# Kernel optimization log

Hardware: AMD Instinct MI355X
Metric: run time of the kernel (lower is better)

The kernel has to match this reference:

```python
import math
import jax, jax.numpy as jnp
import numpy as np

N_TOKENS = 2048
HIDDEN = 2880
HEAD_DIM = 64
N_HEADS = 64          # total attention heads
N_KV = 8              # key/value heads
Q_MULT = N_HEADS // N_KV
SLIDING_WINDOW = 128  # layer_idx=0 (even) -> window active
ROPE_BASE = 150000.0
INIT_CTX = 4096.0
ROPE_SCALE = 32.0
NTK_ALPHA = 1.0
NTK_BETA = 32.0
QKV_DIM = HEAD_DIM * (N_HEADS + 2 * N_KV)  # 5120
EPS = 1e-5
NEG = -1e30


def _cos_sin(n_tokens):
    # YaRN-scaled rotary tables (scaling_factor > 1 branch)
    freq = ROPE_BASE ** (jnp.arange(0, HEAD_DIM, 2, dtype=jnp.float32) / HEAD_DIM)
    concentration = 0.1 * jnp.log(jnp.float32(ROPE_SCALE)) + 1.0
    d_half = HEAD_DIM / 2
    log_base = jnp.log(jnp.float32(ROPE_BASE))
    low = d_half * jnp.log(jnp.float32(INIT_CTX / (NTK_BETA * 2 * np.pi))) / log_base
    high = d_half * jnp.log(jnp.float32(INIT_CTX / (NTK_ALPHA * 2 * np.pi))) / log_base
    interpolation = 1.0 / (ROPE_SCALE * freq)
    extrapolation = 1.0 / freq
    ramp = (jnp.arange(d_half, dtype=jnp.float32) - low) / (high - low)
    mask = 1.0 - jnp.clip(ramp, 0.0, 1.0)
    inv_freq = interpolation * (1.0 - mask) + extrapolation * mask
    t = jnp.arange(n_tokens, dtype=jnp.float32)
    freqs = t[:, None] * inv_freq[None, :]          # [n, head_dim//2]
    return jnp.cos(freqs) * concentration, jnp.sin(freqs) * concentration


def _apply_rotary(x, cos, sin):
    # x: [n, heads, head_dim]; cos/sin: [n, head_dim//2]
    cos = cos[:, None, :].astype(x.dtype)
    sin = sin[:, None, :].astype(x.dtype)
    x1, x2 = jnp.split(x, 2, axis=-1)
    return jnp.concatenate((x1 * cos - x2 * sin, x2 * cos + x1 * sin), axis=-1)


def _rmsnorm(x, scale):
    t = x.astype(jnp.float32)
    rms = jnp.sqrt(jnp.mean(t * t, axis=-1, keepdims=True) + EPS)
    return (t / rms * scale).astype(x.dtype)


def _sdpa(q, k, v, sinks):
    # q: [n, h_kv, q_mult, d]; k, v: [n, h_kv, d]; sinks: [n_heads]
    n = q.shape[0]
    sm_scale = 1.0 / math.sqrt(HEAD_DIM)
    q32, k32, v32 = q.astype(jnp.float32), k.astype(jnp.float32), v.astype(jnp.float32)
    qk = jnp.einsum('qhmd,khd->hmqk', q32, k32) * jnp.float32(sm_scale)
    i = jnp.arange(n)
    # causal AND within sliding window: q - window < k <= q
    allowed = (i[None, :] <= i[:, None]) & (i[None, :] > i[:, None] - SLIDING_WINDOW)
    qk = qk + jnp.where(allowed, jnp.float32(0.0), jnp.float32(NEG))[None, None, :, :]
    s = sinks.astype(jnp.float32).reshape(N_KV, Q_MULT, 1, 1)
    s = jnp.broadcast_to(s, (N_KV, Q_MULT, n, 1))
    w = jax.nn.softmax(jnp.concatenate([qk, s], axis=-1), axis=-1)[..., :-1]
    attn = jnp.einsum('hmqk,khd->qhmd', w, v32)
    return attn.astype(q.dtype).reshape(n, -1)  # [n, n_heads*head_dim]


def setup_inputs() -> dict:
    key = jax.random.key(0)
    ks = jax.random.split(key, 5)
    s = 0.02
    return {
        'x': jax.random.normal(ks[0], (N_TOKENS, HIDDEN), jnp.float32),
        'norm_scale': jnp.ones((HIDDEN,), jnp.float32),
        'w_qkv': jax.random.normal(ks[1], (HIDDEN, QKV_DIM), jnp.float32) * s,
        'b_qkv': jnp.zeros((QKV_DIM,), jnp.float32),
        'sinks': jax.random.normal(ks[2], (N_HEADS,), jnp.float32),
        'w_out': jax.random.normal(ks[3], (N_HEADS * HEAD_DIM, HIDDEN), jnp.float32) * s,
        'b_out': jnp.zeros((HIDDEN,), jnp.float32),
    }


def reference(x, norm_scale, w_qkv, b_qkv, sinks, w_out, b_out):
    n = x.shape[0]
    t = _rmsnorm(x, norm_scale)
    qkv = t @ w_qkv + b_qkv                                   # [n, qkv_dim]
    q_end = N_HEADS * HEAD_DIM
    k_end = q_end + N_KV * HEAD_DIM
    q = qkv[:, :q_end].reshape(n, N_KV, Q_MULT, HEAD_DIM)
    k = qkv[:, q_end:k_end].reshape(n, N_KV, HEAD_DIM)
    v = qkv[:, k_end:].reshape(n, N_KV, HEAD_DIM)
    cos, sin = _cos_sin(n)
    q = _apply_rotary(q.reshape(n, -1, HEAD_DIM), cos, sin).reshape(n, N_KV, Q_MULT, HEAD_DIM)
    k = _apply_rotary(k, cos, sin)
    attn = _sdpa(q, k, v, sinks)                              # [n, n_heads*head_dim]
    return x + (attn @ w_out + b_out)
```

## Files before the change

### kernel.cpp

```cpp
#include <hip/hip_runtime.h>
#include <hip/hip_bf16.h>
#include <math.h>

#define N_TOK 2048
#define HIDDEN 2880
#define QKV_DIM 5120
#define LOG2E 1.44269504088896340736f

typedef __attribute__((ext_vector_type(8))) short short8;
typedef __attribute__((ext_vector_type(4))) float f32x4;
typedef __attribute__((ext_vector_type(16))) float f32x16;

__device__ __forceinline__ float bf2f(unsigned short u) {
  union { unsigned int i; float f; } c; c.i = ((unsigned int)u) << 16; return c.f;
}
__device__ __forceinline__ unsigned short f2bf(float f) {
  union { float f; unsigned int i; } c; c.f = f;
  unsigned int i = c.i;
  return (unsigned short)((i + 0x7FFFu + ((i >> 16) & 1u)) >> 16);
}
__device__ __forceinline__ void gload16(const void* g, void* l) {
  __builtin_amdgcn_global_load_lds((const __attribute__((address_space(1))) void*)g,
                                   (__attribute__((address_space(3))) void*)l, 16, 0, 0);
}

__global__ __launch_bounds__(256) void prep_kernel(
    const float* __restrict__ w_qkv, unsigned short* __restrict__ wqkvT,
    const float* __restrict__ w_out, unsigned short* __restrict__ woutT,
    const float* __restrict__ x, const float* __restrict__ scale,
    unsigned short* __restrict__ t_bf,
    float* __restrict__ cstab, float* __restrict__ sntab)
{
  __shared__ float tile[64][65];
  int b = blockIdx.x;
  const int t = threadIdx.x;
  if (b >= 8528) {
    const float log_base = 11.9183905731f;
    const float low  = 32.f * logf(4096.f / (32.f * 6.283185307179586f)) / log_base;
    const float high = 32.f * logf(4096.f / 6.283185307179586f) / log_base;
    const float conc = 1.3465735903f;
    int e0 = (b - 8528) * 1024 + t * 4;
#pragma unroll
    for (int k = 0; k < 4; ++k) {
      int entry = e0 + k;
      int token = entry >> 5, d = entry & 31;
      float fj = (float)d;
      float extrap = expf(-log_base * fj * 0.03125f);
      float interp = extrap * 0.03125f;
      float ramp = (fj - low) / (high - low);
      float maskv = 1.f - fminf(fmaxf(ramp, 0.f), 1.f);
      float inv_freq = interp * (1.f - maskv) + extrap * maskv;
      float ang = (float)token * inv_freq;
      float s, c;
      sincosf(ang, &s, &c);
      cstab[entry] = c * conc;
      sntab[entry] = s * conc;
    }
    return;
  }
  if (b >= 6480) {
    int row = b - 6480;
    const float* xr = x + (size_t)row * HIDDEN;
    float ss = 0.f;
    for (int i = t; i < HIDDEN / 4; i += 256) {
      float4 v = ((const float4*)xr)[i];
      ss += v.x * v.x + v.y * v.y + v.z * v.z + v.w * v.w;
    }
#pragma unroll
    for (int off = 32; off; off >>= 1) ss += __shfl_down(ss, off, 64);
    __shared__ float red[4];
    if ((t & 63) == 0) red[t >> 6] = ss;
    __syncthreads();
    float total = red[0] + red[1] + red[2] + red[3];
    float rinv = rsqrtf(total / (float)HIDDEN + 1e-5f);
    for (int i = t; i < HIDDEN / 4; i += 256) {
      float4 v = ((const float4*)xr)[i];
      float4 s4 = ((const float4*)scale)[i];
      union { unsigned short u[4]; uint2 p; } pk;
      pk.u[0] = f2bf(v.x * rinv * s4.x);
      pk.u[1] = f2bf(v.y * rinv * s4.y);
      pk.u[2] = f2bf(v.z * rinv * s4.z);
      pk.u[3] = f2bf(v.w * rinv * s4.w);
      *(uint2*)&t_bf[(size_t)row * HIDDEN + i * 4] = pk.p;
    }
    return;
  }
  const float* in; unsigned short* out; int R, C, bx, by;
  if (b < 3600) { in = w_qkv; out = wqkvT; R = 2880; C = 5120; bx = b % 80; by = b / 80; }
  else { b -= 3600; in = w_out; out = woutT; R = 4096; C = 2880; bx = b % 45; by = b / 45; }
  const int r0 = by * 64, c0 = bx * 64;
  const int c4 = t & 15, rr = t >> 4;
#pragma unroll
  for (int p = 0; p < 4; ++p) {
    int row = rr + p * 16;
    float4 v = *(const float4*)&in[(size_t)(r0 + row) * C + c0 + c4 * 4];
    tile[row][c4 * 4 + 0] = v.x; tile[row][c4 * 4 + 1] = v.y;
    tile[row][c4 * 4 + 2] = v.z; tile[row][c4 * 4 + 3] = v.w;
  }
  __syncthreads();
  const int rc = t & 7;
#pragma unroll
  for (int it = 0; it < 2; ++it) {
    int cc = (t >> 3) + it * 32;
    unsigned short tmp[8];
#pragma unroll
    for (int i = 0; i < 8; ++i) tmp[i] = f2bf(tile[rc * 8 + i][cc]);
    *(uint4*)&out[(size_t)(c0 + cc) * R + r0 + rc * 8] = *(uint4*)tmp;
  }
}

template <int NF, int EPI>
__global__ __launch_bounds__(512, 2) void gemm8(
    const unsigned short* __restrict__ A,
    const unsigned short* __restrict__ Bt,
    const float* __restrict__ bias,
    const float* __restrict__ resid,
    void* __restrict__ Cout,
    int K, int Ncols)
{
  constexpr int BUFSZ = 16384 + NF * 8192;
  constexpr int NCH = 2 + NF;
  constexpr int HALF = NCH / 2;
  __shared__ char smem_[2 * BUFSZ];
  const int tid = threadIdx.x;
  const int lane = tid & 63;
  const int w = tid >> 6;
  const int fr = lane & 15, fq = lane >> 4;
  const int wr = w >> 2, wc = w & 3;

  const int nwg = gridDim.x;
  const int cpx = nwg >> 3;
  const int wg = (blockIdx.x & 7) * cpx + (blockIdx.x >> 3);
  const int by = wg & 15, bx = wg >> 4;
  const int row0 = by * 128, col0 = bx * (NF * 64);

  const unsigned short* gsrc[NCH];
  int ldsoff[NCH];
#pragma unroll
  for (int c = 0; c < NCH; ++c) {
    int g = tid + 512 * c;
    if (g < 1024) {
      int kk = g >> 9, rr = (g >> 2) & 127, u = g & 3;
      gsrc[c] = A + (size_t)(row0 + rr) * K + kk * 32 + ((u ^ ((rr >> 1) & 3)) * 8);
      ldsoff[c] = kk * 8192 + rr * 64 + u * 16;
    } else {
      int g2 = g - 1024;
      int kk = g2 / (NF * 256);
      int rm = g2 - kk * (NF * 256);
      int rr = rm >> 2, u = rm & 3;
      gsrc[c] = Bt + (size_t)(col0 + rr) * K + kk * 32 + ((u ^ ((rr >> 1) & 3)) * 8);
      ldsoff[c] = 16384 + kk * (NF * 4096) + rr * 64 + u * 16;
    }
  }
  const int urd = (fq ^ ((fr >> 1) & 3)) * 16;
  const int aoffb = (wr * 64 + fr) * 64 + urd;
  const int boffb = 16384 + (wc * NF * 16 + fr) * 64 + urd;

  f32x4 acc[4][NF];
#pragma unroll
  for (int mf = 0; mf < 4; ++mf)
#pragma unroll
    for (int nf = 0; nf < NF; ++nf) acc[mf][nf] = (f32x4)0.f;

  const int NT = K >> 6;

#define ISSUE(c) gload16(gsrc[c] + ktn, smem_ + nbufo + ldsoff[c])
#define RD_A(mf, kk) (*(const short8*)(smem_ + bufo + (kk)*8192 + (mf)*1024 + aoffb))
#define RD_B(nf, kk) (*(const short8*)(smem_ + bufo + (kk)*(NF*4096) + (nf)*1024 + boffb))

  {
    const int ktn = 0, nbufo = 0;
#pragma unroll
    for (int c = 0; c < NCH; ++c) gload16(gsrc[c] + ktn, smem_ + nbufo + ldsoff[c]);
  }

  for (int t = 0; t < NT; ++t) {
    const int bufo = (t & 1) * BUFSZ;
    const int nbufo = bufo ^ BUFSZ;
    const int ktn = (t + 1) * 64;
    const bool pref = (t + 1) < NT;

    asm volatile("s_waitcnt vmcnt(0)" ::: "memory");
    __builtin_amdgcn_s_barrier();

    if (pref) {
#pragma unroll
      for (int c = 0; c < HALF; ++c) ISSUE(c);
    }

    short8 afr[4], bfr[NF];
#pragma unroll
    for (int nf = 0; nf < NF; ++nf) bfr[nf] = RD_B(nf, 0);
#pragma unroll
    for (int mf = 0; mf < 4; ++mf) afr[mf] = RD_A(mf, 0);
    __builtin_amdgcn_s_setprio(1);
#pragma unroll
    for (int mf = 0; mf < 4; ++mf)
#pragma unroll
      for (int nf = 0; nf < NF; ++nf)
        acc[mf][nf] = __builtin_amdgcn_mfma_f32_16x16x32_bf16(afr[mf], bfr[nf], acc[mf][nf], 0, 0, 0);
    __builtin_amdgcn_s_setprio(0);

    if (pref) {
#pragma unroll
      for (int c = HALF; c < NCH; ++c) ISSUE(c);
    }

#pragma unroll
    for (int nf = 0; nf < NF; ++nf) bfr[nf] = RD_B(nf, 1);
#pragma unroll
    for (int mf = 0; mf < 4; ++mf) afr[mf] = RD_A(mf, 1);
    __builtin_amdgcn_s_setprio(1);
#pragma unroll
    for (int mf = 0; mf < 4; ++mf)
#pragma unroll
      for (int nf = 0; nf < NF; ++nf)
        acc[mf][nf] = __builtin_amdgcn_mfma_f32_16x16x32_bf16(afr[mf], bfr[nf], acc[mf][nf], 0, 0, 0);
    __builtin_amdgcn_s_setprio(0);
  }
#undef ISSUE
#undef RD_A
#undef RD_B

#pragma unroll
  for (int mf = 0; mf < 4; ++mf) {
#pragma unroll
    for (int nf = 0; nf < NF; ++nf) {
      const int colb = col0 + wc * NF * 16 + nf * 16 + fr;
      const int rowb = row0 + wr * 64 + mf * 16 + fq * 4;
      const float bs = bias[colb];
      if (EPI == 1) {
#pragma unroll
        for (int j = 0; j < 4; ++j)
          ((unsigned short*)Cout)[(size_t)(rowb + j) * Ncols + colb] =
              f2bf(acc[mf][nf][j] + bs);
      } else {
#pragma unroll
        for (int j = 0; j < 4; ++j) {
          const size_t idx = (size_t)(rowb + j) * Ncols + colb;
          ((float*)Cout)[idx] = acc[mf][nf][j] + bs + resid[idx];
        }
      }
    }
  }
}

__global__ __launch_bounds__(512, 2) void gemm_d3(
    const unsigned short* __restrict__ A,
    const unsigned short* __restrict__ Bt,
    const float* __restrict__ bias,
    const float* __restrict__ resid,
    float* __restrict__ Cout,
    int K, int Ncols)
{
  constexpr int NF = 3;
  constexpr int BUFSZ = 16384 + NF * 8192;
  constexpr int NCH = 2 + NF;
  __shared__ char smem_[3 * BUFSZ];
  const int tid = threadIdx.x;
  const int lane = tid & 63;
  const int w = tid >> 6;
  const int fr = lane & 15, fq = lane >> 4;
  const int wr = w >> 2, wc = w & 3;

  const int nwg = gridDim.x;
  const int cpx = nwg >> 3;
  const int wg = (blockIdx.x & 7) * cpx + (blockIdx.x >> 3);
  const int by = wg & 15, bx = wg >> 4;
  const int row0 = by * 128, col0 = bx * (NF * 64);

  const unsigned short* gsrc[NCH];
  int ldsoff[NCH];
#pragma unroll
  for (int c = 0; c < NCH; ++c) {
    int g = tid + 512 * c;
    if (g < 1024) {
      int kk = g >> 9, rr = (g >> 2) & 127, u = g & 3;
      gsrc[c] = A + (size_t)(row0 + rr) * K + kk * 32 + ((u ^ ((rr >> 1) & 3)) * 8);
      ldsoff[c] = kk * 8192 + rr * 64 + u * 16;
    } else {
      int g2 = g - 1024;
      int kk = g2 / (NF * 256);
      int rm = g2 - kk * (NF * 256);
      int rr = rm >> 2, u = rm & 3;
      gsrc[c] = Bt + (size_t)(col0 + rr) * K + kk * 32 + ((u ^ ((rr >> 1) & 3)) * 8);
      ldsoff[c] = 16384 + kk * (NF * 4096) + rr * 64 + u * 16;
    }
  }
  const int urd = (fq ^ ((fr >> 1) & 3)) * 16;
  const int aoffb = (wr * 64 + fr) * 64 + urd;
  const int boffb = 16384 + (wc * NF * 16 + fr) * 64 + urd;

  f32x4 acc[4][NF];
#pragma unroll
  for (int mf = 0; mf < 4; ++mf)
#pragma unroll
    for (int nf = 0; nf < NF; ++nf) acc[mf][nf] = (f32x4)0.f;

  const int NT = K >> 6;

#define RD_A(mf, kk) (*(const short8*)(smem_ + bufo + (kk)*8192 + (mf)*1024 + aoffb))
#define RD_B(nf, kk) (*(const short8*)(smem_ + bufo + (kk)*(NF*4096) + (nf)*1024 + boffb))

#pragma unroll
  for (int c = 0; c < NCH; ++c) gload16(gsrc[c], smem_ + ldsoff[c]);
#pragma unroll
  for (int c = 0; c < NCH; ++c) gload16(gsrc[c] + 64, smem_ + BUFSZ + ldsoff[c]);

  int bcur = 0;
  for (int t = 0; t < NT; ++t) {
    const int bufo = bcur * BUFSZ;

    if (t < NT - 1) asm volatile("s_waitcnt vmcnt(5)" ::: "memory");
    else            asm volatile("s_waitcnt vmcnt(0)" ::: "memory");
    __builtin_amdgcn_s_barrier();

    if (t + 2 < NT) {
      int b2 = bcur + 2; if (b2 >= 3) b2 -= 3;
      const int nbufo = b2 * BUFSZ;
      const int ktn = (t + 2) * 64;
#pragma unroll
      for (int c = 0; c < NCH; ++c) gload16(gsrc[c] + ktn, smem_ + nbufo + ldsoff[c]);
    }

    short8 afr[4], bfr[NF];
#pragma unroll
    for (int nf = 0; nf < NF; ++nf) bfr[nf] = RD_B(nf, 0);
#pragma unroll
    for (int mf = 0; mf < 4; ++mf) afr[mf] = RD_A(mf, 0);
    __builtin_amdgcn_s_setprio(1);
#pragma unroll
    for (int mf = 0; mf < 4; ++mf)
#pragma unroll
      for (int nf = 0; nf < NF; ++nf)
        acc[mf][nf] = __builtin_amdgcn_mfma_f32_16x16x32_bf16(afr[mf], bfr[nf], acc[mf][nf], 0, 0, 0);
    __builtin_amdgcn_s_setprio(0);
#pragma unroll
    for (int nf = 0; nf < NF; ++nf) bfr[nf] = RD_B(nf, 1);
#pragma unroll
    for (int mf = 0; mf < 4; ++mf) afr[mf] = RD_A(mf, 1);
    __builtin_amdgcn_s_setprio(1);
#pragma unroll
    for (int mf = 0; mf < 4; ++mf)
#pragma unroll
      for (int nf = 0; nf < NF; ++nf)
        acc[mf][nf] = __builtin_amdgcn_mfma_f32_16x16x32_bf16(afr[mf], bfr[nf], acc[mf][nf], 0, 0, 0);
    __builtin_amdgcn_s_setprio(0);

    bcur = (bcur + 1 == 3) ? 0 : bcur + 1;
  }
#undef RD_A
#undef RD_B

#pragma unroll
  for (int mf = 0; mf < 4; ++mf) {
#pragma unroll
    for (int nf = 0; nf < NF; ++nf) {
      const int colb = col0 + wc * NF * 16 + nf * 16 + fr;
      const int rowb = row0 + wr * 64 + mf * 16 + fq * 4;
      const float bs = bias[colb];
#pragma unroll
      for (int j = 0; j < 4; ++j) {
        const size_t idx = (size_t)(rowb + j) * Ncols + colb;
        Cout[idx] = acc[mf][nf][j] + bs + resid[idx];
      }
    }
  }
}

__global__ __launch_bounds__(512) void attn_kernel(
    const unsigned short* __restrict__ qkv, const float* __restrict__ sinks,
    const float* __restrict__ cstab, const float* __restrict__ sntab,
    unsigned short* __restrict__ attn)
{
  __shared__ unsigned short Ks[160 * 64];
  __shared__ unsigned short Vt[64 * 192];
  const int tid  = threadIdx.x;
  const int lane = tid & 63;
  const int w    = tid >> 6;
  const int qb = blockIdx.x, kvh = blockIdx.y;
  const int q0 = qb * 32;
  const int kb = q0 - 128;
  const int h  = lane >> 5;
  const int ql = lane & 31;

  for (int task = tid; task < 640; task += 512) {
    int r = task >> 2, p = task & 3;
    int j = kb + r; if (j < 0) j = 0;
    const unsigned short* kp = qkv + (size_t)j * QKV_DIM + 4096 + kvh * 64 + p * 8;
    short8 klo = *(const short8*)kp;
    short8 khi = *(const short8*)(kp + 32);
    float cv[8], sv[8];
    *(float4*)&cv[0] = *(const float4*)&cstab[j * 32 + p * 8];
    *(float4*)&cv[4] = *(const float4*)&cstab[j * 32 + p * 8 + 4];
    *(float4*)&sv[0] = *(const float4*)&sntab[j * 32 + p * 8];
    *(float4*)&sv[4] = *(const float4*)&sntab[j * 32 + p * 8 + 4];
    unsigned short nlo[8], nhi[8];
#pragma unroll
    for (int e = 0; e < 8; ++e) {
      float lo = bf2f(((const unsigned short*)&klo)[e]);
      float hi = bf2f(((const unsigned short*)&khi)[e]);
      nlo[e] = f2bf(lo * cv[e] - hi * sv[e]);
      nhi[e] = f2bf(hi * cv[e] + lo * sv[e]);
    }
    *(short8*)&Ks[r * 64 + ((p ^ (r & 7)) * 8)]       = *(short8*)nlo;
    *(short8*)&Ks[r * 64 + (((p + 4) ^ (r & 7)) * 8)] = *(short8*)nhi;
  }
  for (int c = tid; c < 2560; c += 512) {
    int jl = c >> 4;
    int d4 = (c & 15) * 4;
    int j = kb + jl; if (j < 0) j = 0;
    ushort4 v4 = *(const ushort4*)&qkv[(size_t)j * QKV_DIM + 4608 + kvh * 64 + d4];
    const unsigned short* pv = (const unsigned short*)&v4;
#pragma unroll
    for (int t = 0; t < 4; ++t) {
      int d = d4 + t;
      int slot = (jl >> 3) ^ (d & 7);
      Vt[d * 192 + slot * 8 + (jl & 7)] = pv[t];
    }
  }
  const int head = kvh * 8 + w;
  const int i_q = q0 + ql;
  short8 qf[4];
  {
    const unsigned short* qp = qkv + (size_t)i_q * QKV_DIM + head * 64 + h * 8;
#pragma unroll
    for (int ks = 0; ks < 4; ++ks) qf[ks] = *(const short8*)(qp + ks * 16);
#pragma unroll
    for (int p = 0; p < 2; ++p) {
      float cv[8], sv[8];
      int o = i_q * 32 + p * 16 + h * 8;
      *(float4*)&cv[0] = *(const float4*)&cstab[o];
      *(float4*)&cv[4] = *(const float4*)&cstab[o + 4];
      *(float4*)&sv[0] = *(const float4*)&sntab[o];
      *(float4*)&sv[4] = *(const float4*)&sntab[o + 4];
      unsigned short nlo[8], nhi[8];
#pragma unroll
      for (int e = 0; e < 8; ++e) {
        float lo = bf2f(((const unsigned short*)&qf[p])[e]);
        float hi = bf2f(((const unsigned short*)&qf[p + 2])[e]);
        nlo[e] = f2bf(lo * cv[e] - hi * sv[e]);
        nhi[e] = f2bf(hi * cv[e] + lo * sv[e]);
      }
      qf[p]     = *(short8*)nlo;
      qf[p + 2] = *(short8*)nhi;
    }
  }
  __syncthreads();

  const float SC = 0.125f * LOG2E;
  f32x16 oacc0 = (f32x16)(0.f), oacc1 = (f32x16)(0.f);
  float m = -1e30f, l = 0.f;

  const int tstart = qb < 4 ? 4 - qb : 0;
  for (int tt = tstart; tt < 5; ++tt) {
    const int j0 = kb + tt * 32;
    f32x16 sacc = (f32x16)(0.f);
    const int kr = tt * 32 + ql;
#pragma unroll
    for (int ks = 0; ks < 4; ++ks) {
      short8 kf = *(const short8*)&Ks[kr * 64 + (((ks * 2 + h) ^ (kr & 7)) * 8)];
      sacc = __builtin_amdgcn_mfma_f32_32x32x16_bf16(kf, qf[ks], sacc, 0, 0, 0);
    }
    float sc16[16];
    float mt = -INFINITY;
#pragma unroll
    for (int e = 0; e < 16; ++e) {
      int kk = (e & 3) + 8 * (e >> 2) + 4 * h;
      int j = j0 + kk;
      float s2 = sacc[e] * SC;
      bool valid = (j <= i_q) && (j > i_q - 128);
      s2 = valid ? s2 : -INFINITY;
      sc16[e] = s2;
      mt = fmaxf(mt, s2);
    }
    mt = fmaxf(mt, __shfl_xor(mt, 32));
    float mnew = fmaxf(m, mt);
    float r = exp2f(m - mnew);
    l *= r;
    oacc0 *= r;
    oacc1 *= r;
    m = mnew;
    unsigned int wpk[8];
    float ls = 0.f;
#pragma unroll
    for (int e2 = 0; e2 < 8; ++e2) {
      float plo = exp2f(sc16[2 * e2]     - m);
      float phi = exp2f(sc16[2 * e2 + 1] - m);
      ls += plo + phi;
      asm("v_cvt_pk_bf16_f32 %0, %1, %2" : "=v"(wpk[e2]) : "v"(plo), "v"(phi));
    }
    l += ls;
#pragma unroll
    for (int m16 = 0; m16 < 2; ++m16) {
      int go = 2 * m16 + h;
      int gs = 2 * m16 + 1 - h;
      unsigned int x0 = (unsigned int)__shfl_xor((int)wpk[2 * gs],     32);
      unsigned int x1 = (unsigned int)__shfl_xor((int)wpk[2 * gs + 1], 32);
      union { unsigned int u[4]; short8 s; } bu;
      bu.u[0] = h ? x0 : wpk[2 * go];
      bu.u[1] = h ? x1 : wpk[2 * go + 1];
      bu.u[2] = h ? wpk[2 * go]     : x0;
      bu.u[3] = h ? wpk[2 * go + 1] : x1;
      short8 bfrag = bu.s;
#pragma unroll
      for (int dt = 0; dt < 2; ++dt) {
        int d = dt * 32 + ql;
        int slot = (tt * 4 + m16 * 2 + h) ^ (d & 7);
        short8 vf = *(const short8*)&Vt[d * 192 + slot * 8];
        if (dt == 0)
          oacc0 = __builtin_amdgcn_mfma_f32_32x32x16_bf16(vf, bfrag, oacc0, 0, 0, 0);
        else
          oacc1 = __builtin_amdgcn_mfma_f32_32x32x16_bf16(vf, bfrag, oacc1, 0, 0, 0);
      }
    }
  }
  float lt = l + __shfl_xor(l, 32);
  lt += exp2f(sinks[head] * LOG2E - m);
  float inv = 1.f / lt;
  unsigned short* op = attn + (size_t)i_q * 4096 + head * 64;
#pragma unroll
  for (int dt = 0; dt < 2; ++dt) {
#pragma unroll
    for (int g = 0; g < 4; ++g) {
      float f0, f1, f2, f3;
      if (dt == 0) {
        f0 = oacc0[4 * g]; f1 = oacc0[4 * g + 1]; f2 = oacc0[4 * g + 2]; f3 = oacc0[4 * g + 3];
      } else {
        f0 = oacc1[4 * g]; f1 = oacc1[4 * g + 1]; f2 = oacc1[4 * g + 2]; f3 = oacc1[4 * g + 3];
      }
      unsigned int u0, u1;
      asm("v_cvt_pk_bf16_f32 %0, %1, %2" : "=v"(u0) : "v"(f0 * inv), "v"(f1 * inv));
      asm("v_cvt_pk_bf16_f32 %0, %1, %2" : "=v"(u1) : "v"(f2 * inv), "v"(f3 * inv));
      int d = dt * 32 + 8 * g + 4 * h;
      uint2 pr; pr.x = u0; pr.y = u1;
      *(uint2*)(op + d) = pr;
    }
  }
}

extern "C" void kernel_launch(void* const* d_in, const int* in_sizes, int n_in,
                              void* d_out, int out_size, void* d_ws, size_t ws_size,
                              hipStream_t stream)
{
  const float* x      = (const float*)d_in[0];
  const float* nscale = (const float*)d_in[1];
  const float* w_qkv  = (const float*)d_in[2];
  const float* b_qkv  = (const float*)d_in[3];
  const float* sinks  = (const float*)d_in[4];
  const float* w_out  = (const float*)d_in[5];
  const float* b_out  = (const float*)d_in[6];

  char* ws = (char*)d_ws;
  unsigned short* t_bf  = (unsigned short*)(ws);
  unsigned short* wqkvT = (unsigned short*)(ws + 11796480);
  unsigned short* qkv   = (unsigned short*)(ws + 41287680);
  unsigned short* attn  = (unsigned short*)(ws + 62259200);
  unsigned short* woutT = (unsigned short*)(ws + 79036416);
  float* cstab          = (float*)(ws + 102629376);
  float* sntab          = (float*)(ws + 102891520);

  prep_kernel<<<8592, 256, 0, stream>>>(w_qkv, wqkvT, w_out, woutT, x, nscale, t_bf,
                                        cstab, sntab);
  gemm8<5, 1><<<256, 512, 0, stream>>>(t_bf, wqkvT, b_qkv, nullptr, (void*)qkv, 2880, 5120);
  attn_kernel<<<dim3(64, 8), 512, 0, stream>>>(qkv, sinks, cstab, sntab, attn);
  gemm_d3<<<240, 512, 0, stream>>>(attn, woutT, b_out, x, (float*)d_out, 4096, 2880);
}
```

Before: 176.7 us.

## Switch output GEMM to double-buffered K=128 tiles with split prefetch issue

The output projection GEMM moves from a triple-buffered 64-wide K step to a double-buffered 128-wide K step, so it takes half as many barriers and waits. The next tile's A loads and the first B chunk are issued right after the barrier, and the remaining B loads go out after the first MFMA sub-step, spreading global-to-LDS traffic across the compute. The cost is a full vmcnt(0) wait each iteration, with less prefetch depth to hide memory latency. LDS per block rises to about 160KB, which may limit residency to one block per CU despite the occupancy hint of 2.

Result: no change. 175.7 us (-0.5%).

```diff
diff --git a/kernel.cpp b/kernel.cpp
--- a/kernel.cpp
+++ b/kernel.cpp
@@ -245,7 +245,7 @@
   }
 }
 
-__global__ __launch_bounds__(512, 2) void gemm_d3(
+__global__ __launch_bounds__(512, 2) void gemm_o(
     const unsigned short* __restrict__ A,
     const unsigned short* __restrict__ Bt,
     const float* __restrict__ bias,
@@ -254,9 +254,8 @@
     int K, int Ncols)
 {
   constexpr int NF = 3;
-  constexpr int BUFSZ = 16384 + NF * 8192;
-  constexpr int NCH = 2 + NF;
-  __shared__ char smem_[3 * BUFSZ];
+  constexpr int BUFSZ = 32768 + NF * 16384;
+  __shared__ char smem_[2 * BUFSZ];
   const int tid = threadIdx.x;
   const int lane = tid & 63;
   const int w = tid >> 6;
@@ -269,27 +268,29 @@
   const int by = wg & 15, bx = wg >> 4;
   const int row0 = by * 128, col0 = bx * (NF * 64);
 
-  const unsigned short* gsrc[NCH];
-  int ldsoff[NCH];
-#pragma unroll
-  for (int c = 0; c < NCH; ++c) {
+  const unsigned short* gsrcA[4];
+  int loffA[4];
+#pragma unroll
+  for (int c = 0; c < 4; ++c) {
     int g = tid + 512 * c;
-    if (g < 1024) {
-      int kk = g >> 9, rr = (g >> 2) & 127, u = g & 3;
-      gsrc[c] = A + (size_t)(row0 + rr) * K + kk * 32 + ((u ^ ((rr >> 1) & 3)) * 8);
-      ldsoff[c] = kk * 8192 + rr * 64 + u * 16;
-    } else {
-      int g2 = g - 1024;
-      int kk = g2 / (NF * 256);
-      int rm = g2 - kk * (NF * 256);
-      int rr = rm >> 2, u = rm & 3;
-      gsrc[c] = Bt + (size_t)(col0 + rr) * K + kk * 32 + ((u ^ ((rr >> 1) & 3)) * 8);
-      ldsoff[c] = 16384 + kk * (NF * 4096) + rr * 64 + u * 16;
-    }
+    int kk = g >> 9, rr = (g >> 2) & 127, u = g & 3;
+    gsrcA[c] = A + (size_t)(row0 + rr) * K + kk * 32 + ((u ^ ((rr >> 1) & 3)) * 8);
+    loffA[c] = kk * 8192 + rr * 64 + u * 16;
+  }
+  const unsigned short* gsrcB[6];
+  int loffB[6];
+#pragma unroll
+  for (int c = 0; c < 6; ++c) {
+    int g = tid + 512 * c;
+    int kk = g / 768;
+    int rm = g - kk * 768;
+    int rr = rm >> 2, u = rm & 3;
+    gsrcB[c] = Bt + (size_t)(col0 + rr) * K + kk * 32 + ((u ^ ((rr >> 1) & 3)) * 8);
+    loffB[c] = 32768 + kk * 12288 + rr * 64 + u * 16;
   }
   const int urd = (fq ^ ((fr >> 1) & 3)) * 16;
   const int aoffb = (wr * 64 + fr) * 64 + urd;
-  const int boffb = 16384 + (wc * NF * 16 + fr) * 64 + urd;
+  const int boffb = 32768 + (wc * 48 + fr) * 64 + urd;
 
   f32x4 acc[4][NF];
 #pragma unroll
@@ -297,57 +298,50 @@
 #pragma unroll
     for (int nf = 0; nf < NF; ++nf) acc[mf][nf] = (f32x4)0.f;
 
-  const int NT = K >> 6;
+  const int NT = K >> 7;
 
 #define RD_A(mf, kk) (*(const short8*)(smem_ + bufo + (kk)*8192 + (mf)*1024 + aoffb))
-#define RD_B(nf, kk) (*(const short8*)(smem_ + bufo + (kk)*(NF*4096) + (nf)*1024 + boffb))
-
-#pragma unroll
-  for (int c = 0; c < NCH; ++c) gload16(gsrc[c], smem_ + ldsoff[c]);
-#pragma unroll
-  for (int c = 0; c < NCH; ++c) gload16(gsrc[c] + 64, smem_ + BUFSZ + ldsoff[c]);
-
-  int bcur = 0;
+#define RD_B(nf, kk) (*(const short8*)(smem_ + bufo + (kk)*12288 + (nf)*1024 + boffb))
+
+#pragma unroll
+  for (int c = 0; c < 4; ++c) gload16(gsrcA[c], smem_ + loffA[c]);
+#pragma unroll
+  for (int c = 0; c < 6; ++c) gload16(gsrcB[c], smem_ + loffB[c]);
+
   for (int t = 0; t < NT; ++t) {
-    const int bufo = bcur * BUFSZ;
-
-    if (t < NT - 1) asm volatile("s_waitcnt vmcnt(5)" ::: "memory");
-    else            asm volatile("s_waitcnt vmcnt(0)" ::: "memory");
+    const int bufo = (t & 1) * BUFSZ;
+    const int nbufo = bufo ^ BUFSZ;
+    const int ktn = (t + 1) * 128;
+    const bool pref = (t + 1) < NT;
+
+    asm volatile("s_waitcnt vmcnt(0)" ::: "memory");
     __builtin_amdgcn_s_barrier();
 
-    if (t + 2 < NT) {
-      int b2 = bcur + 2; if (b2 >= 3) b2 -= 3;
-      const int nbufo = b2 * BUFSZ;
-      const int ktn = (t + 2) * 64;
-#pragma unroll
-      for (int c = 0; c < NCH; ++c) gload16(gsrc[c] + ktn, smem_ + nbufo + ldsoff[c]);
+    if (pref) {
+#pragma unroll
+      for (int c = 0; c < 4; ++c) gload16(gsrcA[c] + ktn, smem_ + nbufo + loffA[c]);
+      gload16(gsrcB[0] + ktn, smem_ + nbufo + loffB[0]);
     }
 
     short8 afr[4], bfr[NF];
 #pragma unroll
-    for (int nf = 0; nf < NF; ++nf) bfr[nf] = RD_B(nf, 0);
-#pragma unroll
-    for (int mf = 0; mf < 4; ++mf) afr[mf] = RD_A(mf, 0);
-    __builtin_amdgcn_s_setprio(1);
-#pragma unroll
-    for (int mf = 0; mf < 4; ++mf)
-#pragma unroll
-      for (int nf = 0; nf < NF; ++nf)
-        acc[mf][nf] = __builtin_amdgcn_mfma_f32_16x16x32_bf16(afr[mf], bfr[nf], acc[mf][nf], 0, 0, 0);
-    __builtin_amdgcn_s_setprio(0);
-#pragma unroll
-    for (int nf = 0; nf < NF; ++nf) bfr[nf] = RD_B(nf, 1);
-#pragma unroll
-    for (int mf = 0; mf < 4; ++mf) afr[mf] = RD_A(mf, 1);
-    __builtin_amdgcn_s_setprio(1);
-#pragma unroll
-    for (int mf = 0; mf < 4; ++mf)
-#pragma unroll
-      for (int nf = 0; nf < NF; ++nf)
-        acc[mf][nf] = __builtin_amdgcn_mfma_f32_16x16x32_bf16(afr[mf], bfr[nf], acc[mf][nf], 0, 0, 0);
-    __builtin_amdgcn_s_setprio(0);
-
-    bcur = (bcur + 1 == 3) ? 0 : bcur + 1;
+    for (int kk = 0; kk < 4; ++kk) {
+#pragma unroll
+      for (int nf = 0; nf < NF; ++nf) bfr[nf] = RD_B(nf, kk);
+#pragma unroll
+      for (int mf = 0; mf < 4; ++mf) afr[mf] = RD_A(mf, kk);
+      __builtin_amdgcn_s_setprio(1);
+#pragma unroll
+      for (int mf = 0; mf < 4; ++mf)
+#pragma unroll
+        for (int nf = 0; nf < NF; ++nf)
+          acc[mf][nf] = __builtin_amdgcn_mfma_f32_16x16x32_bf16(afr[mf], bfr[nf], acc[mf][nf], 0, 0, 0);
+      __builtin_amdgcn_s_setprio(0);
+      if (kk == 0 && pref) {
+#pragma unroll
+        for (int c = 1; c < 6; ++c) gload16(gsrcB[c] + ktn, smem_ + nbufo + loffB[c]);
+      }
+    }
   }
 #undef RD_A
 #undef RD_B
@@ -564,5 +558,5 @@
                                         cstab, sntab);
   gemm8<5, 1><<<256, 512, 0, stream>>>(t_bf, wqkvT, b_qkv, nullptr, (void*)qkv, 2880, 5120);
   attn_kernel<<<dim3(64, 8), 512, 0, stream>>>(qkv, sinks, cstab, sntab, attn);
-  gemm_d3<<<240, 512, 0, stream>>>(attn, woutT, b_out, x, (float*)d_out, 4096, 2880);
-}
+  gemm_o<<<240, 512, 0, stream>>>(attn, woutT, b_out, x, (float*)d_out, 4096, 2880);
+}
```
